# Kernel optimization log

Hardware: AMD Instinct MI355X
Metric: run time of the kernel (lower is better)

Reference implementation:

```python
import jax, jax.numpy as jnp
import numpy as np

DIM = 384
NUM_HEADS = 12
WS = 8            # window_size
SS = 4            # shift_size
HEAD_DIM = DIM // NUM_HEADS
SCALE = HEAD_DIM ** -0.5
N = WS * WS       # tokens per window
EPS = 1e-5
MLP_HIDDEN = 4 * DIM

# relative position index (static, matches torch buffer construction)
_coords = np.stack(np.meshgrid(np.arange(WS), np.arange(WS), indexing='ij')).reshape(2, -1)
_rel = (_coords[:, :, None] - _coords[:, None, :]).transpose(1, 2, 0)  # [N,N,2]
_rel[..., 0] += WS - 1
_rel[..., 1] += WS - 1
_rel[..., 0] *= 2 * WS - 1
RPI = jnp.asarray(_rel.sum(-1))  # [N,N] int


def layer_norm(x, g, b):
    m = x.mean(-1, keepdims=True)
    v = ((x - m) ** 2).mean(-1, keepdims=True)
    return (x - m) / jnp.sqrt(v + EPS) * g + b


def window_partition(x):
    B, Hh, Ww, C = x.shape
    x = x.reshape(B, Hh // WS, WS, Ww // WS, WS, C).transpose(0, 1, 3, 2, 4, 5)
    return x.reshape(-1, WS, WS, C)


def window_reverse(w, Hh, Ww):
    B = w.shape[0] // ((Hh // WS) * (Ww // WS))
    x = w.reshape(B, Hh // WS, Ww // WS, WS, WS, -1).transpose(0, 1, 3, 2, 4, 5)
    return x.reshape(B, Hh, Ww, -1)


def attention_mask(Hp, Wp):
    # region id along each axis: 0 = [0, Hp-WS), 1 = [Hp-WS, Hp-SS), 2 = [Hp-SS, Hp)
    h_id = np.zeros(Hp, np.int32); h_id[Hp - WS:Hp - SS] = 1; h_id[Hp - SS:] = 2
    w_id = np.zeros(Wp, np.int32); w_id[Wp - WS:Wp - SS] = 1; w_id[Wp - SS:] = 2
    cnt = h_id[:, None] * 3 + w_id[None, :]                      # [Hp, Wp]
    img = jnp.asarray(cnt, jnp.float32).reshape(1, Hp, Wp, 1)
    mw = window_partition(img).reshape(-1, N)                    # [nW, N]
    am = mw[:, None, :] - mw[:, :, None]                         # [nW, N, N]
    return jnp.where(am != 0, jnp.float32(-100.0), jnp.float32(0.0))


def setup_inputs() -> dict:
    key = jax.random.key(0)
    ks = jax.random.split(key, 8)
    B, H, W = 32, 64, 64
    std = 0.02
    return {
        'x': jax.random.normal(ks[0], (B, H * W, DIM), jnp.float32),
        'qkv_w': jax.random.normal(ks[1], (DIM, 3 * DIM), jnp.float32) * std,
        'qkv_b': jnp.zeros((3 * DIM,), jnp.float32),
        'proj_w': jax.random.normal(ks[2], (DIM, DIM), jnp.float32) * std,
        'proj_b': jnp.zeros((DIM,), jnp.float32),
        'rpb_table': jax.random.normal(ks[3], ((2 * WS - 1) * (2 * WS - 1), NUM_HEADS), jnp.float32) * std,
        'n1_g': jnp.ones((DIM,), jnp.float32), 'n1_b': jnp.zeros((DIM,), jnp.float32),
        'n2_g': jnp.ones((DIM,), jnp.float32), 'n2_b': jnp.zeros((DIM,), jnp.float32),
        'fc1_w': jax.random.normal(ks[4], (DIM, MLP_HIDDEN), jnp.float32) * std,
        'fc1_b': jnp.zeros((MLP_HIDDEN,), jnp.float32),
        'fc2_w': jax.random.normal(ks[5], (MLP_HIDDEN, DIM), jnp.float32) * std,
        'fc2_b': jnp.zeros((DIM,), jnp.float32),
        'H': 64, 'W': 64,
    }


def reference(x, qkv_w, qkv_b, proj_w, proj_b, rpb_table, n1_g, n1_b, n2_g, n2_b,
              fc1_w, fc1_b, fc2_w, fc2_b, H, W):
    B, L, C = x.shape
    shortcut = x
    h = layer_norm(x, n1_g, n1_b).reshape(B, H, W, C)
    pad_r = (WS - W % WS) % WS
    pad_b = (WS - H % WS) % WS
    if pad_r or pad_b:
        h = jnp.pad(h, ((0, 0), (0, pad_b), (0, pad_r), (0, 0)))
    Hp, Wp = H + pad_b, W + pad_r
    shifted = jnp.roll(h, shift=(-SS, -SS), axis=(1, 2))
    xw = window_partition(shifted).reshape(-1, N, C)             # [B_, N, C]
    B_ = xw.shape[0]

    qkv = (xw @ qkv_w + qkv_b).reshape(B_, N, 3, NUM_HEADS, HEAD_DIM)
    q = qkv[:, :, 0].transpose(0, 2, 1, 3) * SCALE               # [B_, h, N, d]
    k = qkv[:, :, 1].transpose(0, 2, 1, 3)
    v = qkv[:, :, 2].transpose(0, 2, 1, 3)

    attn = jnp.einsum('bhnd,bhmd->bhnm', q, k)                   # [B_, h, N, N]
    bias = rpb_table[RPI].transpose(2, 0, 1)                     # [h, N, N]
    attn = attn + bias[None]

    mask = attention_mask(Hp, Wp)                                # [nW, N, N]
    nW = mask.shape[0]
    attn = attn.reshape(B_ // nW, nW, NUM_HEADS, N, N) + mask[None, :, None]
    attn = jax.nn.softmax(attn.reshape(B_, NUM_HEADS, N, N), axis=-1)

    out = jnp.einsum('bhnm,bhmd->bhnd', attn, v)
    out = out.transpose(0, 2, 1, 3).reshape(B_, N, C)
    out = out @ proj_w + proj_b

    out = window_reverse(out.reshape(-1, WS, WS, C), Hp, Wp)
    out = jnp.roll(out, shift=(SS, SS), axis=(1, 2))
    out = out[:, :H, :W, :].reshape(B, H * W, C)

    x = shortcut + out
    h2 = layer_norm(x, n2_g, n2_b)
    mlp = jax.nn.gelu(h2 @ fc1_w + fc1_b, approximate=False) @ fc2_w + fc2_b
    return x + mlp
```

## Files before the change

kernel.cpp:

```cpp
#include <hip/hip_runtime.h>
#include <math.h>


#define ROWS_TOTAL 131072
#define NWIN_TOTAL 2048

typedef __attribute__((ext_vector_type(8))) __bf16 bf16x8;
typedef __attribute__((ext_vector_type(4))) float f32x4;
typedef __attribute__((ext_vector_type(8))) unsigned short ushort8;

__device__ __forceinline__ unsigned short f2bf(float f) {
  unsigned u = __builtin_bit_cast(unsigned, f);
  u = (u + 0x7fffu + ((u >> 16) & 1u)) >> 16;
  return (unsigned short)u;
}
__device__ __forceinline__ float bf2f(unsigned short u) {
  return __builtin_bit_cast(float, (unsigned)u << 16);
}

__device__ __forceinline__ void gload16(const void* g, void* l) {
  __builtin_amdgcn_global_load_lds(
      (const __attribute__((address_space(1))) unsigned int*)g,
      (__attribute__((address_space(3))) unsigned int*)l, 16, 0, 0);
}

__device__ __forceinline__ int gather_row(int win, int t) {
  int b = win >> 6, wi = (win >> 3) & 7, wj = win & 7;
  int gi = (wi * 8 + (t >> 3) + 4) & 63;
  int gj = (wj * 8 + (t & 7) + 4) & 63;
  return (b << 12) + (gi << 6) + gj;
}

#define LGK0() asm volatile("s_waitcnt lgkmcnt(0)" ::: "memory")
#define VM6() asm volatile("s_waitcnt vmcnt(6)" ::: "memory")
#define VM0() asm volatile("s_waitcnt vmcnt(0)" ::: "memory")
#define SCB() __builtin_amdgcn_sched_barrier(0)
#define BARR() __builtin_amdgcn_s_barrier()
#define PRIO1() __builtin_amdgcn_s_setprio(1)
#define PRIO0() __builtin_amdgcn_s_setprio(0)


#define STGA(b_, c_, kt_)                                                   \
  gload16(aSrcC[c_] + (size_t)(kt_) * 64,                                   \
          (char*)&As[0][0] + (b_) * 32768 + (c_) * 8192 + w * 1024)
#define STGB(b_, c_, kt_)                                                   \
  gload16(bSrcC[c_] + (size_t)(kt_) * 64,                                   \
          (char*)&Bs[0][0] + (b_) * 16384 + (c_) * 8192 + w * 1024)

#define LDA(mi_)                                                            \
  { a[mi_][0] = *(const bf16x8*)(AsB + aOff[mi_][0]);                       \
    a[mi_][1] = *(const bf16x8*)(AsB + aOff[mi_][1]); }
#define LDB(nj_)                                                            \
  { b[nj_][0] = *(const bf16x8*)(BsB + bOff[nj_][0]);                       \
    b[nj_][1] = *(const bf16x8*)(BsB + bOff[nj_][1]); }
#define MM(mi_, nj_)                                                        \
  { acc[mi_][nj_] = __builtin_amdgcn_mfma_f32_16x16x32_bf16(                \
        a[mi_][0], b[nj_][0], acc[mi_][nj_], 0, 0, 0);                      \
    acc[mi_][nj_] = __builtin_amdgcn_mfma_f32_16x16x32_bf16(                \
        a[mi_][1], b[nj_][1], acc[mi_][nj_], 0, 0, 0); }

#define GEMM_DECLS()                                                        \
  f32x4 acc[4][4];                                                          \
  bf16x8 a[4][2], b[4][2];                                                  \
  int aOff[4][2], bOff[4][2];                                               \
  _Pragma("unroll") for (int i_ = 0; i_ < 4; ++i_)                          \
  _Pragma("unroll") for (int j_ = 0; j_ < 4; ++j_)                          \
      acc[i_][j_] = (f32x4)(0.f);                                           \
  _Pragma("unroll") for (int mi_ = 0; mi_ < 4; ++mi_)                       \
  _Pragma("unroll") for (int ks_ = 0; ks_ < 2; ++ks_) {                     \
    int sl_ = ((ks_ * 4 + hi) ^ (lr & 7)) * 8;                              \
    aOff[mi_][ks_] = (wr * 64 + mi_ * 16 + lr) * 64 + sl_;                  \
    bOff[mi_][ks_] = (wc * 64 + mi_ * 16 + lr) * 64 + sl_;                  \
  }

#define GEMM_CORE(NT)                                                       \
  {                                                                         \
    STGA(0, 0, 0); STGA(0, 1, 0); STGA(0, 2, 0); STGA(0, 3, 0);             \
    STGB(0, 0, 0); STGB(0, 1, 0);                                           \
    STGA(1, 0, 1); STGA(1, 1, 1); STGA(1, 2, 1); STGA(1, 3, 1);             \
    STGB(1, 0, 1); STGB(1, 1, 1);                                           \
    VM6(); SCB(); BARR(); SCB();                                            \
    for (int t = 0; t < (NT); ++t) {                                        \
      const int cur = t % 3, nxt = (t + 2) % 3;                             \
      const bool st = (t + 2) < (NT);                                       \
      const int kt = t + 2;                                                 \
      const ushort* AsB = &As[0][0] + cur * 16384;                          \
      const ushort* BsB = &Bs[0][0] + cur * 8192;                           \
                                                                    \
      LDA(0); LDA(1); LDB(0); LDB(1);                                       \
      if (st) { STGA(nxt, 0, kt); STGA(nxt, 1, kt); }                       \
      SCB(); BARR(); LGK0(); SCB();                                         \
      PRIO1(); MM(0, 0); MM(0, 1); MM(1, 0); MM(1, 1); PRIO0();             \
      SCB(); BARR(); SCB();                                                 \
                                                                    \
      LDB(2); LDB(3);                                                       \
      if (st) { STGA(nxt, 2, kt); STGA(nxt, 3, kt); }                       \
      SCB(); BARR(); LGK0(); SCB();                                         \
      PRIO1(); MM(0, 2); MM(0, 3); MM(1, 2); MM(1, 3); PRIO0();             \
      SCB(); BARR(); SCB();                                                 \
                                                                    \
      LDA(2); LDA(3);                                                       \
      if (st) { STGB(nxt, 0, kt); }                                         \
      SCB(); BARR(); LGK0(); SCB();                                         \
      PRIO1(); MM(2, 2); MM(2, 3); MM(3, 2); MM(3, 3); PRIO0();             \
      SCB(); BARR(); SCB();                                                 \
                                                                    \
      if (st) { STGB(nxt, 1, kt); }                                         \
      PRIO1(); MM(2, 0); MM(2, 1); MM(3, 0); MM(3, 1); PRIO0();             \
      if (st) { VM6(); } else { VM0(); }                                    \
      SCB(); BARR(); SCB();                                                 \
    }                                                                       \
  }

__global__ __launch_bounds__(256) void wprep_k(
    const float* __restrict__ qkvw, const float* __restrict__ projw,
    const float* __restrict__ fc1w, const float* __restrict__ fc2w,
    ushort* __restrict__ wq, ushort* __restrict__ wp,
    ushort* __restrict__ w1, ushort* __restrict__ w2) {
  int gid = blockIdx.x * 256 + threadIdx.x;
  const int S1 = 1152 * 384;
  const int S2 = S1 + 384 * 384;
  const int S3 = S2 + 1536 * 384;
  const int S4 = S3 + 384 * 1536;
  if (gid < S1) {
    int n = gid / 384, k = gid - n * 384;
    wq[gid] = f2bf(qkvw[(size_t)k * 1152 + n]);
  } else if (gid < S2) {
    int i = gid - S1, n = i / 384, k = i - n * 384;
    wp[i] = f2bf(projw[(size_t)k * 384 + n]);
  } else if (gid < S3) {
    int i = gid - S2, n = i / 384, k = i - n * 384;
    w1[i] = f2bf(fc1w[(size_t)k * 1536 + n]);
  } else if (gid < S4) {
    int i = gid - S3, n = i / 1536, k = i - n * 1536;
    w2[i] = f2bf(fc2w[(size_t)k * 384 + n]);
  }
}

__global__ __launch_bounds__(256) void ln_fused_k(
    const float* __restrict__ x, const float* __restrict__ g,
    const float* __restrict__ b, ushort* __restrict__ o) {
  int wid = threadIdx.x >> 6, lane = threadIdx.x & 63;
  int row = (blockIdx.x << 2) + wid;
  const float* p = x + (size_t)row * 384;
  float2 v[3];
  float s = 0.f, ss = 0.f;
#pragma unroll
  for (int c = 0; c < 3; ++c) {
    v[c] = *(const float2*)(p + lane * 2 + c * 128);
    s += v[c].x + v[c].y;
    ss += v[c].x * v[c].x + v[c].y * v[c].y;
  }
#pragma unroll
  for (int off = 1; off < 64; off <<= 1) {
    s += __shfl_xor(s, off);
    ss += __shfl_xor(ss, off);
  }
  float m = s * (1.f / 384.f);
  float r = rsqrtf(ss * (1.f / 384.f) - m * m + 1e-5f);
  ushort* op = o + (size_t)row * 384;
#pragma unroll
  for (int c = 0; c < 3; ++c) {
    float2 gg = *(const float2*)(g + lane * 2 + c * 128);
    float2 bb = *(const float2*)(b + lane * 2 + c * 128);
    union { ushort u[2]; unsigned w; } pk;
    pk.u[0] = f2bf((v[c].x - m) * r * gg.x + bb.x);
    pk.u[1] = f2bf((v[c].y - m) * r * gg.y + bb.y);
    *(unsigned*)(op + lane * 2 + c * 128) = pk.w;
  }
}

__global__ __launch_bounds__(512, 2) void qkv_mfma_k(
    const ushort* __restrict__ xln, const ushort* __restrict__ wq,
    const float* __restrict__ qkvb, ushort* __restrict__ qd,
    ushort* __restrict__ kd, ushort* __restrict__ vd, int wc0) {
  __shared__ __align__(16) ushort As[3][16384];
  __shared__ __align__(16) ushort Bs[3][8192];
  __shared__ int rowS[256];
  const int tid = threadIdx.x;
  const int w = tid >> 6, lane = tid & 63;
  const int wr = w >> 1, wc = w & 1;
  int p, bm;
  {
    int lin = blockIdx.y * 9 + blockIdx.x;
    if ((gridDim.y & 7) == 0) {
      int xcd = lin & 7, q = lin >> 3;
      p = q % 9; bm = (q / 9) * 8 + xcd;
    } else { p = blockIdx.x; bm = blockIdx.y; }
  }
  const int n0 = p * 128;
  if (tid < 256) rowS[tid] = gather_row(wc0 + bm * 4 + (tid >> 6), tid & 63);
  __syncthreads();
  const int lr = lane & 15, hi = lane >> 4;
  const int swz = ((tid & 7) ^ ((tid >> 3) & 7)) * 8;
  const ushort* aSrcC[4];
  const ushort* bSrcC[2];
#pragma unroll
  for (int c = 0; c < 4; ++c)
    aSrcC[c] = xln + (size_t)rowS[c * 64 + (tid >> 3)] * 384 + swz;
#pragma unroll
  for (int c = 0; c < 2; ++c)
    bSrcC[c] = wq + (size_t)(n0 + c * 64 + (tid >> 3)) * 384 + swz;
  GEMM_DECLS();
  GEMM_CORE(6);
  const float scale = 0.17677669529663687f;
#pragma unroll
  for (int mi = 0; mi < 4; ++mi) {
#pragma unroll
    for (int r = 0; r < 4; ++r) {
      int rr = wr * 64 + mi * 16 + (hi << 2) + r;
      int w_rel = bm * 4 + (rr >> 6), t = rr & 63;
#pragma unroll
      for (int nj = 0; nj < 4; ++nj) {
        int nc = n0 + wc * 64 + nj * 16 + lr;
        float v = acc[mi][nj][r] + qkvb[nc];
        int qi = nc / 384, rem = nc - qi * 384;
        int hh = rem >> 5, d = rem & 31;
        ushort* base = (qi == 0) ? qd : (qi == 1 ? kd : vd);
        if (qi == 0) v *= scale;
        base[(((size_t)w_rel * 12 + hh) << 11) + (t << 5) + d] = f2bf(v);
      }
    }
  }
}

__global__ __launch_bounds__(128) void attn_k(
    const ushort* __restrict__ q, const ushort* __restrict__ k,
    const ushort* __restrict__ v, const float* __restrict__ rpb,
    ushort* __restrict__ ao, int wc0) {
  __shared__ __align__(16) float kbuf[2][64][32];
  __shared__ __align__(16) float vbuf[2][64][32];
  __shared__ float bias[2][232];
  __shared__ int region[64];
  const int tid = threadIdx.x;
  const int wid = tid >> 6, lane = tid & 63;
  const int w = blockIdx.x, win = wc0 + w;
  const int head = blockIdx.y * 2 + wid;
  if (tid < 64) {
    int wi = (win >> 3) & 7, wj = win & 7;
    int pi = wi * 8 + (tid >> 3), pj = wj * 8 + (tid & 7);
    int ri = pi < 56 ? 0 : (pi < 60 ? 1 : 2);
    int rj = pj < 56 ? 0 : (pj < 60 ? 1 : 2);
    region[tid] = ri * 3 + rj;
  }
  const size_t hb = ((size_t)w * 12 + head) * 2048;
  const ushort* kp = k + hb;
  const ushort* vp = v + hb;
#pragma unroll
  for (int s = 0; s < 4; ++s) {
    int f = s * 64 + lane;
    int r = f >> 2, c = (f & 3) * 8;
    ushort8 ku = *(const ushort8*)(kp + r * 32 + c);
    ushort8 vu = *(const ushort8*)(vp + r * 32 + c);
#pragma unroll
    for (int j = 0; j < 8; ++j) {
      kbuf[wid][r][c + j] = bf2f(ku[j]);
      vbuf[wid][r][c + j] = bf2f(vu[j]);
    }
  }
  for (int s = lane; s < 225; s += 64) bias[wid][s] = rpb[s * 12 + head];
  __syncthreads();
  const int i = lane;
  float qr[32];
  const ushort* qp = q + hb + (i << 5);
#pragma unroll
  for (int c = 0; c < 4; ++c) {
    ushort8 qu = *(const ushort8*)(qp + c * 8);
#pragma unroll
    for (int j = 0; j < 8; ++j) qr[c * 8 + j] = bf2f(qu[j]);
  }
  const int yi = i >> 3, xi = i & 7, regi = region[i];
  float sc[64];
  float mx = -3.0e38f;
#pragma unroll
  for (int j = 0; j < 64; ++j) {
    float a = 0.f;
#pragma unroll
    for (int c = 0; c < 32; c += 4) {
      float4 kv = *(float4*)&kbuf[wid][j][c];
      a = fmaf(qr[c], kv.x, a);
      a = fmaf(qr[c + 1], kv.y, a);
      a = fmaf(qr[c + 2], kv.z, a);
      a = fmaf(qr[c + 3], kv.w, a);
    }
    int dy = yi - (j >> 3) + 7, dx = xi - (j & 7) + 7;
    a += bias[wid][dy * 15 + dx];
    if (region[j] != regi) a -= 100.f;
    sc[j] = a;
    mx = fmaxf(mx, a);
  }
  float sum = 0.f;
#pragma unroll
  for (int j = 0; j < 64; ++j) {
    float e = __expf(sc[j] - mx);
    sc[j] = e;
    sum += e;
  }
  const float inv = 1.f / sum;
  float o[32];
#pragma unroll
  for (int c = 0; c < 32; ++c) o[c] = 0.f;
#pragma unroll
  for (int j = 0; j < 64; ++j) {
    float p = sc[j];
#pragma unroll
    for (int c = 0; c < 32; c += 4) {
      float4 vv = *(float4*)&vbuf[wid][j][c];
      o[c] = fmaf(p, vv.x, o[c]);
      o[c + 1] = fmaf(p, vv.y, o[c + 1]);
      o[c + 2] = fmaf(p, vv.z, o[c + 2]);
      o[c + 3] = fmaf(p, vv.w, o[c + 3]);
    }
  }
  ushort* op = ao + ((size_t)(w * 64 + i)) * 384 + (head << 5);
#pragma unroll
  for (int c = 0; c < 32; c += 8) {
    ushort8 pk;
#pragma unroll
    for (int j2 = 0; j2 < 8; ++j2) pk[j2] = f2bf(o[c + j2] * inv);
    *(ushort8*)(op + c) = pk;
  }
}

__global__ __launch_bounds__(512, 2) void proj_mfma_k(
    const ushort* __restrict__ ao, const ushort* __restrict__ wp,
    const float* __restrict__ pb, const float* __restrict__ x,
    float* __restrict__ x2, int wc0) {
  __shared__ __align__(16) ushort As[3][16384];
  __shared__ __align__(16) ushort Bs[3][8192];
  const int tid = threadIdx.x;
  const int w = tid >> 6, lane = tid & 63;
  const int wr = w >> 1, wc = w & 1;
  int p, bm;
  {
    int lin = blockIdx.y * 3 + blockIdx.x;
    if ((gridDim.y & 7) == 0) {
      int xcd = lin & 7, q = lin >> 3;
      p = q % 3; bm = (q / 3) * 8 + xcd;
    } else { p = blockIdx.x; bm = blockIdx.y; }
  }
  const int n0 = p * 128;
  const int lr = lane & 15, hi = lane >> 4;
  const int swz = ((tid & 7) ^ ((tid >> 3) & 7)) * 8;
  const ushort* aSrcC[4];
  const ushort* bSrcC[2];
#pragma unroll
  for (int c = 0; c < 4; ++c)
    aSrcC[c] = ao + (size_t)(bm * 256 + c * 64 + (tid >> 3)) * 384 + swz;
#pragma unroll
  for (int c = 0; c < 2; ++c)
    bSrcC[c] = wp + (size_t)(n0 + c * 64 + (tid >> 3)) * 384 + swz;
  GEMM_DECLS();
  GEMM_CORE(6);
#pragma unroll
  for (int mi = 0; mi < 4; ++mi) {
#pragma unroll
    for (int r = 0; r < 4; ++r) {
      int rr = wr * 64 + mi * 16 + (hi << 2) + r;
      int gl = bm * 256 + rr;
      int gr = gather_row(wc0 + (gl >> 6), gl & 63);
#pragma unroll
      for (int nj = 0; nj < 4; ++nj) {
        int nc = n0 + wc * 64 + nj * 16 + lr;
        size_t idx = (size_t)gr * 384 + nc;
        x2[idx] = acc[mi][nj][r] + pb[nc] + x[idx];
      }
    }
  }
}

__global__ __launch_bounds__(512, 2) void fc1_mfma_k(
    const ushort* __restrict__ x2ln, const ushort* __restrict__ w1,
    const float* __restrict__ fb, ushort* __restrict__ hm, int row0) {
  __shared__ __align__(16) ushort As[3][16384];
  __shared__ __align__(16) ushort Bs[3][8192];
  const int tid = threadIdx.x;
  const int w = tid >> 6, lane = tid & 63;
  const int wr = w >> 1, wc = w & 1;
  int p, bm;
  {
    int lin = blockIdx.y * 12 + blockIdx.x;
    if ((gridDim.y & 7) == 0) {
      int xcd = lin & 7, q = lin >> 3;
      p = q % 12; bm = (q / 12) * 8 + xcd;
    } else { p = blockIdx.x; bm = blockIdx.y; }
  }
  const int n0 = p * 128;
  const int lr = lane & 15, hi = lane >> 4;
  const int swz = ((tid & 7) ^ ((tid >> 3) & 7)) * 8;
  const ushort* aSrcC[4];
  const ushort* bSrcC[2];
#pragma unroll
  for (int c = 0; c < 4; ++c)
    aSrcC[c] =
        x2ln + (size_t)(row0 + bm * 256 + c * 64 + (tid >> 3)) * 384 + swz;
#pragma unroll
  for (int c = 0; c < 2; ++c)
    bSrcC[c] = w1 + (size_t)(n0 + c * 64 + (tid >> 3)) * 384 + swz;
  GEMM_DECLS();
  GEMM_CORE(6);
#pragma unroll
  for (int mi = 0; mi < 4; ++mi) {
#pragma unroll
    for (int r = 0; r < 4; ++r) {
      int rr = wr * 64 + mi * 16 + (hi << 2) + r;
      size_t lrow = (size_t)(bm * 256 + rr);
#pragma unroll
      for (int nj = 0; nj < 4; ++nj) {
        int nc = n0 + wc * 64 + nj * 16 + lr;
        float v = acc[mi][nj][r] + fb[nc];
        v = 0.5f * v * (1.f + erff(v * 0.70710678118654752f));
        hm[lrow * 1536 + nc] = f2bf(v);
      }
    }
  }
}

__global__ __launch_bounds__(512, 2) void fc2_mfma_k(
    const ushort* __restrict__ hm, const ushort* __restrict__ w2,
    const float* __restrict__ fb, float* __restrict__ out, int row0) {
  __shared__ __align__(16) ushort As[3][16384];
  __shared__ __align__(16) ushort Bs[3][8192];
  const int tid = threadIdx.x;
  const int w = tid >> 6, lane = tid & 63;
  const int wr = w >> 1, wc = w & 1;
  int p, bm;
  {
    int lin = blockIdx.y * 3 + blockIdx.x;
    if ((gridDim.y & 7) == 0) {
      int xcd = lin & 7, q = lin >> 3;
      p = q % 3; bm = (q / 3) * 8 + xcd;
    } else { p = blockIdx.x; bm = blockIdx.y; }
  }
  const int n0 = p * 128;
  const int lr = lane & 15, hi = lane >> 4;
  const int swz = ((tid & 7) ^ ((tid >> 3) & 7)) * 8;
  const ushort* aSrcC[4];
  const ushort* bSrcC[2];
#pragma unroll
  for (int c = 0; c < 4; ++c)
    aSrcC[c] = hm + (size_t)(bm * 256 + c * 64 + (tid >> 3)) * 1536 + swz;
#pragma unroll
  for (int c = 0; c < 2; ++c)
    bSrcC[c] = w2 + (size_t)(n0 + c * 64 + (tid >> 3)) * 1536 + swz;
  GEMM_DECLS();
  GEMM_CORE(24);
#pragma unroll
  for (int mi = 0; mi < 4; ++mi) {
#pragma unroll
    for (int r = 0; r < 4; ++r) {
      int rr = wr * 64 + mi * 16 + (hi << 2) + r;
      size_t grow = (size_t)(row0 + bm * 256 + rr);
#pragma unroll
      for (int nj = 0; nj < 4; ++nj) {
        int nc = n0 + wc * 64 + nj * 16 + lr;
        size_t idx = grow * 384 + nc;
        out[idx] = out[idx] + acc[mi][nj][r] + fb[nc];
      }
    }
  }
}

extern "C" void kernel_launch(void* const* d_in, const int* in_sizes, int n_in,
                              void* d_out, int out_size, void* d_ws, size_t ws_size,
                              hipStream_t stream) {
  const float* x = (const float*)d_in[0];
  const float* qkv_w = (const float*)d_in[1];
  const float* qkv_b = (const float*)d_in[2];
  const float* proj_w = (const float*)d_in[3];
  const float* proj_b = (const float*)d_in[4];
  const float* rpb = (const float*)d_in[5];
  const float* n1g = (const float*)d_in[6];
  const float* n1b = (const float*)d_in[7];
  const float* n2g = (const float*)d_in[8];
  const float* n2b = (const float*)d_in[9];
  const float* fc1w = (const float*)d_in[10];
  const float* fc1b = (const float*)d_in[11];
  const float* fc2w = (const float*)d_in[12];
  const float* fc2b = (const float*)d_in[13];
  float* out = (float*)d_out;
  char* ws = (char*)d_ws;

  ushort* wq = (ushort*)ws;
  ushort* wp = wq + 442368;
  ushort* w1 = wp + 147456;
  ushort* w2 = w1 + 589824;
  ushort* xln = (ushort*)(ws + 3538944);
  char* scratch = ws + 3538944 + 100663296;
  size_t base = 3538944 + 100663296;
  size_t ssz = (ws_size > base) ? ws_size - base : 0;

  wprep_k<<<6912, 256, 0, stream>>>(qkv_w, proj_w, fc1w, fc2w, wq, wp, w1, w2);
  ln_fused_k<<<ROWS_TOTAL / 4, 256, 0, stream>>>(x, n1g, n1b, xln);

  const size_t perwin = 196608;
  int nwc = (int)(ssz / perwin);
  if (nwc > NWIN_TOTAL) nwc = NWIN_TOTAL;
  nwc &= ~3;
  if (nwc < 4) nwc = 4;
  ushort* qd = (ushort*)scratch;
  ushort* kd = qd + (size_t)nwc * 24576;
  ushort* vd = kd + (size_t)nwc * 24576;
  ushort* ao = vd + (size_t)nwc * 24576;
  for (int wc0 = 0; wc0 < NWIN_TOTAL; wc0 += nwc) {
    int nw = (NWIN_TOTAL - wc0 < nwc) ? (NWIN_TOTAL - wc0) : nwc;
    qkv_mfma_k<<<dim3(9, nw / 4), 512, 0, stream>>>(xln, wq, qkv_b, qd, kd, vd, wc0);
    attn_k<<<dim3(nw, 6), 128, 0, stream>>>(qd, kd, vd, rpb, ao, wc0);
    proj_mfma_k<<<dim3(3, nw / 4), 512, 0, stream>>>(ao, wp, proj_b, x, out, wc0);
  }

  ln_fused_k<<<ROWS_TOTAL / 4, 256, 0, stream>>>(out, n2g, n2b, xln);
  const size_t pergrp = 786432;
  int ngc = (int)(ssz / pergrp);
  if (ngc > 512) ngc = 512;
  ngc &= ~7;
  if (ngc < 8) ngc = 8;
  ushort* hm = (ushort*)scratch;
  for (int g0 = 0; g0 < 512; g0 += ngc) {
    int ng = (512 - g0 < ngc) ? (512 - g0) : ngc;
    fc1_mfma_k<<<dim3(12, ng), 512, 0, stream>>>(xln, w1, fc1b, hm, g0 * 256);
    fc2_mfma_k<<<dim3(3, ng), 512, 0, stream>>>(hm, w2, fc2b, out, g0 * 256);
  }
}
```

Baseline: 1.414 ms.

## Retile GEMMs to 256x192 blocks with 2x4 warp grid and double-buffered B

All four MFMA GEMM kernels move from 256x128 output tiles on a 4x2 warp layout to 256x192 tiles on a 2x4 layout. Each warp now holds 128x48 accumulators and reuses B fragments across eight A sub-tiles. B uses a two-stage LDS buffer, A keeps three stages, the pipeline has fewer barriers per k-step, and grid sizes shrink to match. The exact erf in the fc1 GELU is swapped for a polynomial approximation, and the qkv gather-row shared table is replaced by computing the row index directly. The larger accumulator footprint raises register pressure, and the min-blocks hint is dropped, which risks lower occupancy.

```diff
diff --git a/kernel.cpp b/kernel.cpp
--- a/kernel.cpp
+++ b/kernel.cpp
@@ -31,85 +31,134 @@
   return (b << 12) + (gi << 6) + gj;
 }
 
+__device__ __forceinline__ float gelu_f(float v) {
+  float x = v * 0.70710678118654752f;
+  float ax = fabsf(x);
+  float t = 1.f / (1.f + 0.3275911f * ax);
+  float poly =
+      t * (0.254829592f +
+           t * (-0.284496736f +
+                t * (1.421413741f + t * (-1.453152027f + t * 1.061405429f))));
+  float er = 1.f - poly * __expf(-x * x);
+  er = copysignf(er, x);
+  return 0.5f * v * (1.f + er);
+}
+
 #define LGK0() asm volatile("s_waitcnt lgkmcnt(0)" ::: "memory")
-#define VM6() asm volatile("s_waitcnt vmcnt(6)" ::: "memory")
+#define VM4() asm volatile("s_waitcnt vmcnt(4)" ::: "memory")
 #define VM0() asm volatile("s_waitcnt vmcnt(0)" ::: "memory")
 #define SCB() __builtin_amdgcn_sched_barrier(0)
 #define BARR() __builtin_amdgcn_s_barrier()
 #define PRIO1() __builtin_amdgcn_s_setprio(1)
 #define PRIO0() __builtin_amdgcn_s_setprio(0)
 
-
-#define STGA(b_, c_, kt_)                                                   \
-  gload16(aSrcC[c_] + (size_t)(kt_) * 64,                                   \
-          (char*)&As[0][0] + (b_) * 32768 + (c_) * 8192 + w * 1024)
-#define STGB(b_, c_, kt_)                                                   \
-  gload16(bSrcC[c_] + (size_t)(kt_) * 64,                                   \
-          (char*)&Bs[0][0] + (b_) * 16384 + (c_) * 8192 + w * 1024)
-
-#define LDA(mi_)                                                            \
-  { a[mi_][0] = *(const bf16x8*)(AsB + aOff[mi_][0]);                       \
-    a[mi_][1] = *(const bf16x8*)(AsB + aOff[mi_][1]); }
-#define LDB(nj_)                                                            \
-  { b[nj_][0] = *(const bf16x8*)(BsB + bOff[nj_][0]);                       \
-    b[nj_][1] = *(const bf16x8*)(BsB + bOff[nj_][1]); }
-#define MM(mi_, nj_)                                                        \
-  { acc[mi_][nj_] = __builtin_amdgcn_mfma_f32_16x16x32_bf16(                \
-        a[mi_][0], b[nj_][0], acc[mi_][nj_], 0, 0, 0);                      \
-    acc[mi_][nj_] = __builtin_amdgcn_mfma_f32_16x16x32_bf16(                \
-        a[mi_][1], b[nj_][1], acc[mi_][nj_], 0, 0, 0); }
-
-#define GEMM_DECLS()                                                        \
-  f32x4 acc[4][4];                                                          \
-  bf16x8 a[4][2], b[4][2];                                                  \
-  int aOff[4][2], bOff[4][2];                                               \
-  _Pragma("unroll") for (int i_ = 0; i_ < 4; ++i_)                          \
-  _Pragma("unroll") for (int j_ = 0; j_ < 4; ++j_)                          \
-      acc[i_][j_] = (f32x4)(0.f);                                           \
-  _Pragma("unroll") for (int mi_ = 0; mi_ < 4; ++mi_)                       \
-  _Pragma("unroll") for (int ks_ = 0; ks_ < 2; ++ks_) {                     \
-    int sl_ = ((ks_ * 4 + hi) ^ (lr & 7)) * 8;                              \
-    aOff[mi_][ks_] = (wr * 64 + mi_ * 16 + lr) * 64 + sl_;                  \
-    bOff[mi_][ks_] = (wc * 64 + mi_ * 16 + lr) * 64 + sl_;                  \
-  }
-
-#define GEMM_CORE(NT)                                                       \
-  {                                                                         \
-    STGA(0, 0, 0); STGA(0, 1, 0); STGA(0, 2, 0); STGA(0, 3, 0);             \
-    STGB(0, 0, 0); STGB(0, 1, 0);                                           \
-    STGA(1, 0, 1); STGA(1, 1, 1); STGA(1, 2, 1); STGA(1, 3, 1);             \
-    STGB(1, 0, 1); STGB(1, 1, 1);                                           \
-    VM6(); SCB(); BARR(); SCB();                                            \
-    for (int t = 0; t < (NT); ++t) {                                        \
-      const int cur = t % 3, nxt = (t + 2) % 3;                             \
-      const bool st = (t + 2) < (NT);                                       \
-      const int kt = t + 2;                                                 \
-      const ushort* AsB = &As[0][0] + cur * 16384;                          \
-      const ushort* BsB = &Bs[0][0] + cur * 8192;                           \
-                                                                    \
-      LDA(0); LDA(1); LDB(0); LDB(1);                                       \
-      if (st) { STGA(nxt, 0, kt); STGA(nxt, 1, kt); }                       \
-      SCB(); BARR(); LGK0(); SCB();                                         \
-      PRIO1(); MM(0, 0); MM(0, 1); MM(1, 0); MM(1, 1); PRIO0();             \
-      SCB(); BARR(); SCB();                                                 \
-                                                                    \
-      LDB(2); LDB(3);                                                       \
-      if (st) { STGA(nxt, 2, kt); STGA(nxt, 3, kt); }                       \
-      SCB(); BARR(); LGK0(); SCB();                                         \
-      PRIO1(); MM(0, 2); MM(0, 3); MM(1, 2); MM(1, 3); PRIO0();             \
-      SCB(); BARR(); SCB();                                                 \
-                                                                    \
-      LDA(2); LDA(3);                                                       \
-      if (st) { STGB(nxt, 0, kt); }                                         \
-      SCB(); BARR(); LGK0(); SCB();                                         \
-      PRIO1(); MM(2, 2); MM(2, 3); MM(3, 2); MM(3, 3); PRIO0();             \
-      SCB(); BARR(); SCB();                                                 \
-                                                                    \
-      if (st) { STGB(nxt, 1, kt); }                                         \
-      PRIO1(); MM(2, 0); MM(2, 1); MM(3, 0); MM(3, 1); PRIO0();             \
-      if (st) { VM6(); } else { VM0(); }                                    \
-      SCB(); BARR(); SCB();                                                 \
-    }                                                                       \
+#define STGA_(buf_, kt_, c_)                                          \
+  gload16(aSrcC[c_] + (size_t)(kt_) * 64,                             \
+          (char*)As + (buf_) * 32768 + (c_) * 8192 + w * 1024)
+#define STGB_(buf_, kt_, c_)                                          \
+  gload16(bSrcC[c_] + (size_t)(kt_) * 64,                             \
+          (char*)Bs + (buf_) * 24576 + (c_) * 8192 + w * 1024)
+
+#define MM3(mi_, a_, bs_)                                             \
+  { acc[mi_][0] = __builtin_amdgcn_mfma_f32_16x16x32_bf16(            \
+        a_, bs_[0], acc[mi_][0], 0, 0, 0);                            \
+    acc[mi_][1] = __builtin_amdgcn_mfma_f32_16x16x32_bf16(            \
+        a_, bs_[1], acc[mi_][1], 0, 0, 0);                            \
+    acc[mi_][2] = __builtin_amdgcn_mfma_f32_16x16x32_bf16(            \
+        a_, bs_[2], acc[mi_][2], 0, 0, 0); }
+
+#define GEMM_DECLS()                                                  \
+  f32x4 acc[8][3];                                                    \
+  _Pragma("unroll") for (int i_ = 0; i_ < 8; ++i_)                    \
+  _Pragma("unroll") for (int j_ = 0; j_ < 3; ++j_)                    \
+      acc[i_][j_] = (f32x4)(0.f);                                     \
+  const int sl0 = ((hi) ^ (lr & 7)) * 8;                              \
+  const int sl1 = ((4 + hi) ^ (lr & 7)) * 8;                          \
+  const int aB0 = (wr * 128 + lr) * 64 + sl0;                         \
+  const int aB1 = (wr * 128 + lr) * 64 + sl1;                         \
+  const int bB0 = (wc * 48 + lr) * 64 + sl0;                          \
+  const int bB1 = (wc * 48 + lr) * 64 + sl1;
+
+#define GEMM_CORE(NT_)                                                \
+  {                                                                   \
+    STGA_(0, 0, 0); STGA_(0, 0, 1); STGA_(0, 0, 2); STGA_(0, 0, 3);   \
+    STGB_(0, 0, 0); STGB_(0, 0, 1); STGB_(0, 0, 2);                   \
+    STGA_(1, 1, 0); STGA_(1, 1, 1); STGA_(1, 1, 2); STGA_(1, 1, 3);   \
+    VM4(); SCB(); BARR(); SCB();                                      \
+    int curA = 0;                                                     \
+    for (int t = 0; t < (NT_); ++t) {                                 \
+      const int curB = t & 1;                                         \
+      const ushort* AsC = (const ushort*)As + curA * 16384;           \
+      const ushort* BsC = (const ushort*)Bs + curB * 12288;           \
+      if (t + 1 < (NT_)) {                                            \
+        STGB_(curB ^ 1, t + 1, 0);                                    \
+        STGB_(curB ^ 1, t + 1, 1);                                    \
+        STGB_(curB ^ 1, t + 1, 2);                                    \
+      }                                                               \
+      SCB();                                                          \
+      bf16x8 av0, av1, av2, av3, bv0[3], bv1[3];                      \
+      bv0[0] = *(const bf16x8*)(BsC + bB0);                           \
+      bv0[1] = *(const bf16x8*)(BsC + bB0 + 1024);                    \
+      bv0[2] = *(const bf16x8*)(BsC + bB0 + 2048);                    \
+      bv1[0] = *(const bf16x8*)(BsC + bB1);                           \
+      bv1[1] = *(const bf16x8*)(BsC + bB1 + 1024);                    \
+      bv1[2] = *(const bf16x8*)(BsC + bB1 + 2048);                    \
+      av0 = *(const bf16x8*)(AsC + aB0);                              \
+      av1 = *(const bf16x8*)(AsC + aB0 + 1024);                       \
+      av2 = *(const bf16x8*)(AsC + aB0 + 2048);                       \
+      av3 = *(const bf16x8*)(AsC + aB0 + 3072);                       \
+      LGK0(); SCB();                                                  \
+      PRIO1();                                                        \
+      MM3(0, av0, bv0); MM3(1, av1, bv0);                             \
+      MM3(2, av2, bv0); MM3(3, av3, bv0);                             \
+      PRIO0(); SCB();                                                 \
+      av0 = *(const bf16x8*)(AsC + aB1);                              \
+      av1 = *(const bf16x8*)(AsC + aB1 + 1024);                       \
+      av2 = *(const bf16x8*)(AsC + aB1 + 2048);                       \
+      av3 = *(const bf16x8*)(AsC + aB1 + 3072);                       \
+      LGK0(); SCB();                                                  \
+      PRIO1();                                                        \
+      MM3(0, av0, bv1); MM3(1, av1, bv1);                             \
+      MM3(2, av2, bv1); MM3(3, av3, bv1);                             \
+      PRIO0(); SCB();                                                 \
+      if (t + 2 < (NT_)) {                                            \
+        int nbA = curA + 2; if (nbA >= 3) nbA -= 3;                   \
+        STGA_(nbA, t + 2, 0); STGA_(nbA, t + 2, 1);                   \
+        STGA_(nbA, t + 2, 2); STGA_(nbA, t + 2, 3);                   \
+      }                                                               \
+      SCB();                                                          \
+      av0 = *(const bf16x8*)(AsC + aB0 + 4096);                       \
+      av1 = *(const bf16x8*)(AsC + aB0 + 5120);                       \
+      av2 = *(const bf16x8*)(AsC + aB0 + 6144);                       \
+      av3 = *(const bf16x8*)(AsC + aB0 + 7168);                       \
+      LGK0(); SCB();                                                  \
+      PRIO1();                                                        \
+      MM3(4, av0, bv0); MM3(5, av1, bv0);                             \
+      MM3(6, av2, bv0); MM3(7, av3, bv0);                             \
+      PRIO0(); SCB();                                                 \
+      av0 = *(const bf16x8*)(AsC + aB1 + 4096);                       \
+      av1 = *(const bf16x8*)(AsC + aB1 + 5120);                       \
+      av2 = *(const bf16x8*)(AsC + aB1 + 6144);                       \
+      av3 = *(const bf16x8*)(AsC + aB1 + 7168);                       \
+      LGK0(); SCB();                                                  \
+      PRIO1();                                                        \
+      MM3(4, av0, bv1); MM3(5, av1, bv1);                             \
+      MM3(6, av2, bv1); MM3(7, av3, bv1);                             \
+      PRIO0();                                                        \
+      if (t + 2 < (NT_)) { VM4(); SCB(); BARR(); SCB(); }             \
+      else if (t + 1 < (NT_)) { VM0(); SCB(); BARR(); SCB(); }        \
+      ++curA; if (curA == 3) curA = 0;                                \
+    }                                                                 \
+  }
+
+#define GRID_SWZ(NP_)                                                 \
+  int p, bm;                                                          \
+  {                                                                   \
+    int lin = blockIdx.y * (NP_) + blockIdx.x;                        \
+    if ((gridDim.y & 7) == 0) {                                       \
+      int xcd = lin & 7, q = lin >> 3;                                \
+      p = q % (NP_); bm = (q / (NP_)) * 8 + xcd;                      \
+    } else { p = blockIdx.x; bm = blockIdx.y; }                       \
   }
 
 __global__ __launch_bounds__(256) void wprep_k(
@@ -170,49 +219,40 @@
   }
 }
 
-__global__ __launch_bounds__(512, 2) void qkv_mfma_k(
+__global__ __launch_bounds__(512) void qkv_mfma_k(
     const ushort* __restrict__ xln, const ushort* __restrict__ wq,
     const float* __restrict__ qkvb, ushort* __restrict__ qd,
     ushort* __restrict__ kd, ushort* __restrict__ vd, int wc0) {
   __shared__ __align__(16) ushort As[3][16384];
-  __shared__ __align__(16) ushort Bs[3][8192];
-  __shared__ int rowS[256];
+  __shared__ __align__(16) ushort Bs[2][12288];
   const int tid = threadIdx.x;
   const int w = tid >> 6, lane = tid & 63;
-  const int wr = w >> 1, wc = w & 1;
-  int p, bm;
-  {
-    int lin = blockIdx.y * 9 + blockIdx.x;
-    if ((gridDim.y & 7) == 0) {
-      int xcd = lin & 7, q = lin >> 3;
-      p = q % 9; bm = (q / 9) * 8 + xcd;
-    } else { p = blockIdx.x; bm = blockIdx.y; }
-  }
-  const int n0 = p * 128;
-  if (tid < 256) rowS[tid] = gather_row(wc0 + bm * 4 + (tid >> 6), tid & 63);
-  __syncthreads();
+  const int wr = w >> 2, wc = w & 3;
   const int lr = lane & 15, hi = lane >> 4;
-  const int swz = ((tid & 7) ^ ((tid >> 3) & 7)) * 8;
+  GRID_SWZ(6);
+  const int n0 = p * 192;
+  const int sg = ((tid & 7) ^ ((tid >> 3) & 7)) * 8;
   const ushort* aSrcC[4];
-  const ushort* bSrcC[2];
+  const ushort* bSrcC[3];
 #pragma unroll
   for (int c = 0; c < 4; ++c)
-    aSrcC[c] = xln + (size_t)rowS[c * 64 + (tid >> 3)] * 384 + swz;
-#pragma unroll
-  for (int c = 0; c < 2; ++c)
-    bSrcC[c] = wq + (size_t)(n0 + c * 64 + (tid >> 3)) * 384 + swz;
+    aSrcC[c] =
+        xln + (size_t)gather_row(wc0 + bm * 4 + c, tid >> 3) * 384 + sg;
+#pragma unroll
+  for (int c = 0; c < 3; ++c)
+    bSrcC[c] = wq + (size_t)(n0 + c * 64 + (tid >> 3)) * 384 + sg;
   GEMM_DECLS();
   GEMM_CORE(6);
   const float scale = 0.17677669529663687f;
 #pragma unroll
-  for (int mi = 0; mi < 4; ++mi) {
+  for (int mi = 0; mi < 8; ++mi) {
 #pragma unroll
     for (int r = 0; r < 4; ++r) {
-      int rr = wr * 64 + mi * 16 + (hi << 2) + r;
+      int rr = wr * 128 + mi * 16 + (hi << 2) + r;
       int w_rel = bm * 4 + (rr >> 6), t = rr & 63;
 #pragma unroll
-      for (int nj = 0; nj < 4; ++nj) {
-        int nc = n0 + wc * 64 + nj * 16 + lr;
+      for (int nj = 0; nj < 3; ++nj) {
+        int nc = n0 + wc * 48 + nj * 16 + lr;
         float v = acc[mi][nj][r] + qkvb[nc];
         int qi = nc / 384, rem = nc - qi * 384;
         int hh = rem >> 5, d = rem & 31;
@@ -322,46 +362,39 @@
   }
 }
 
-__global__ __launch_bounds__(512, 2) void proj_mfma_k(
+__global__ __launch_bounds__(512) void proj_mfma_k(
     const ushort* __restrict__ ao, const ushort* __restrict__ wp,
     const float* __restrict__ pb, const float* __restrict__ x,
     float* __restrict__ x2, int wc0) {
   __shared__ __align__(16) ushort As[3][16384];
-  __shared__ __align__(16) ushort Bs[3][8192];
+  __shared__ __align__(16) ushort Bs[2][12288];
   const int tid = threadIdx.x;
   const int w = tid >> 6, lane = tid & 63;
-  const int wr = w >> 1, wc = w & 1;
-  int p, bm;
-  {
-    int lin = blockIdx.y * 3 + blockIdx.x;
-    if ((gridDim.y & 7) == 0) {
-      int xcd = lin & 7, q = lin >> 3;
-      p = q % 3; bm = (q / 3) * 8 + xcd;
-    } else { p = blockIdx.x; bm = blockIdx.y; }
-  }
-  const int n0 = p * 128;
+  const int wr = w >> 2, wc = w & 3;
   const int lr = lane & 15, hi = lane >> 4;
-  const int swz = ((tid & 7) ^ ((tid >> 3) & 7)) * 8;
+  GRID_SWZ(2);
+  const int n0 = p * 192;
+  const int sg = ((tid & 7) ^ ((tid >> 3) & 7)) * 8;
   const ushort* aSrcC[4];
-  const ushort* bSrcC[2];
+  const ushort* bSrcC[3];
 #pragma unroll
   for (int c = 0; c < 4; ++c)
-    aSrcC[c] = ao + (size_t)(bm * 256 + c * 64 + (tid >> 3)) * 384 + swz;
-#pragma unroll
-  for (int c = 0; c < 2; ++c)
-    bSrcC[c] = wp + (size_t)(n0 + c * 64 + (tid >> 3)) * 384 + swz;
+    aSrcC[c] = ao + (size_t)(bm * 256 + c * 64 + (tid >> 3)) * 384 + sg;
+#pragma unroll
+  for (int c = 0; c < 3; ++c)
+    bSrcC[c] = wp + (size_t)(n0 + c * 64 + (tid >> 3)) * 384 + sg;
   GEMM_DECLS();
   GEMM_CORE(6);
 #pragma unroll
-  for (int mi = 0; mi < 4; ++mi) {
+  for (int mi = 0; mi < 8; ++mi) {
 #pragma unroll
     for (int r = 0; r < 4; ++r) {
-      int rr = wr * 64 + mi * 16 + (hi << 2) + r;
+      int rr = wr * 128 + mi * 16 + (hi << 2) + r;
       int gl = bm * 256 + rr;
       int gr = gather_row(wc0 + (gl >> 6), gl & 63);
 #pragma unroll
-      for (int nj = 0; nj < 4; ++nj) {
-        int nc = n0 + wc * 64 + nj * 16 + lr;
+      for (int nj = 0; nj < 3; ++nj) {
+        int nc = n0 + wc * 48 + nj * 16 + lr;
         size_t idx = (size_t)gr * 384 + nc;
         x2[idx] = acc[mi][nj][r] + pb[nc] + x[idx];
       }
@@ -369,91 +402,76 @@
   }
 }
 
-__global__ __launch_bounds__(512, 2) void fc1_mfma_k(
+__global__ __launch_bounds__(512) void fc1_mfma_k(
     const ushort* __restrict__ x2ln, const ushort* __restrict__ w1,
     const float* __restrict__ fb, ushort* __restrict__ hm, int row0) {
   __shared__ __align__(16) ushort As[3][16384];
-  __shared__ __align__(16) ushort Bs[3][8192];
+  __shared__ __align__(16) ushort Bs[2][12288];
   const int tid = threadIdx.x;
   const int w = tid >> 6, lane = tid & 63;
-  const int wr = w >> 1, wc = w & 1;
-  int p, bm;
-  {
-    int lin = blockIdx.y * 12 + blockIdx.x;
-    if ((gridDim.y & 7) == 0) {
-      int xcd = lin & 7, q = lin >> 3;
-      p = q % 12; bm = (q / 12) * 8 + xcd;
-    } else { p = blockIdx.x; bm = blockIdx.y; }
-  }
-  const int n0 = p * 128;
+  const int wr = w >> 2, wc = w & 3;
   const int lr = lane & 15, hi = lane >> 4;
-  const int swz = ((tid & 7) ^ ((tid >> 3) & 7)) * 8;
+  GRID_SWZ(8);
+  const int n0 = p * 192;
+  const int sg = ((tid & 7) ^ ((tid >> 3) & 7)) * 8;
   const ushort* aSrcC[4];
-  const ushort* bSrcC[2];
+  const ushort* bSrcC[3];
 #pragma unroll
   for (int c = 0; c < 4; ++c)
     aSrcC[c] =
-        x2ln + (size_t)(row0 + bm * 256 + c * 64 + (tid >> 3)) * 384 + swz;
-#pragma unroll
-  for (int c = 0; c < 2; ++c)
-    bSrcC[c] = w1 + (size_t)(n0 + c * 64 + (tid >> 3)) * 384 + swz;
+        x2ln + (size_t)(row0 + bm * 256 + c * 64 + (tid >> 3)) * 384 + sg;
+#pragma unroll
+  for (int c = 0; c < 3; ++c)
+    bSrcC[c] = w1 + (size_t)(n0 + c * 64 + (tid >> 3)) * 384 + sg;
   GEMM_DECLS();
   GEMM_CORE(6);
 #pragma unroll
-  for (int mi = 0; mi < 4; ++mi) {
+  for (int mi = 0; mi < 8; ++mi) {
 #pragma unroll
     for (int r = 0; r < 4; ++r) {
-      int rr = wr * 64 + mi * 16 + (hi << 2) + r;
+      int rr = wr * 128 + mi * 16 + (hi << 2) + r;
       size_t lrow = (size_t)(bm * 256 + rr);
 #pragma unroll
-      for (int nj = 0; nj < 4; ++nj) {
-        int nc = n0 + wc * 64 + nj * 16 + lr;
-        float v = acc[mi][nj][r] + fb[nc];
-        v = 0.5f * v * (1.f + erff(v * 0.70710678118654752f));
+      for (int nj = 0; nj < 3; ++nj) {
+        int nc = n0 + wc * 48 + nj * 16 + lr;
+        float v = gelu_f(acc[mi][nj][r] + fb[nc]);
         hm[lrow * 1536 + nc] = f2bf(v);
       }
     }
   }
 }
 
-__global__ __launch_bounds__(512, 2) void fc2_mfma_k(
+__global__ __launch_bounds__(512) void fc2_mfma_k(
     const ushort* __restrict__ hm, const ushort* __restrict__ w2,
     const float* __restrict__ fb, float* __restrict__ out, int row0) {
   __shared__ __align__(16) ushort As[3][16384];
-  __shared__ __align__(16) ushort Bs[3][8192];
+  __shared__ __align__(16) ushort Bs[2][12288];
   const int tid = threadIdx.x;
   const int w = tid >> 6, lane = tid & 63;
-  const int wr = w >> 1, wc = w & 1;
-  int p, bm;
-  {
-    int lin = blockIdx.y * 3 + blockIdx.x;
-    if ((gridDim.y & 7) == 0) {
-      int xcd = lin & 7, q = lin >> 3;
-      p = q % 3; bm = (q / 3) * 8 + xcd;
-    } else { p = blockIdx.x; bm = blockIdx.y; }
-  }
-  const int n0 = p * 128;
+  const int wr = w >> 2, wc = w & 3;
   const int lr = lane & 15, hi = lane >> 4;
-  const int swz = ((tid & 7) ^ ((tid >> 3) & 7)) * 8;
+  GRID_SWZ(2);
+  const int n0 = p * 192;
+  const int sg = ((tid & 7) ^ ((tid >> 3) & 7)) * 8;
   const ushort* aSrcC[4];
-  const ushort* bSrcC[2];
+  const ushort* bSrcC[3];
 #pragma unroll
   for (int c = 0; c < 4; ++c)
-    aSrcC[c] = hm + (size_t)(bm * 256 + c * 64 + (tid >> 3)) * 1536 + swz;
-#pragma unroll
-  for (int c = 0; c < 2; ++c)
-    bSrcC[c] = w2 + (size_t)(n0 + c * 64 + (tid >> 3)) * 1536 + swz;
+    aSrcC[c] = hm + (size_t)(bm * 256 + c * 64 + (tid >> 3)) * 1536 + sg;
+#pragma unroll
+  for (int c = 0; c < 3; ++c)
+    bSrcC[c] = w2 + (size_t)(n0 + c * 64 + (tid >> 3)) * 1536 + sg;
   GEMM_DECLS();
   GEMM_CORE(24);
 #pragma unroll
-  for (int mi = 0; mi < 4; ++mi) {
+  for (int mi = 0; mi < 8; ++mi) {
 #pragma unroll
     for (int r = 0; r < 4; ++r) {
-      int rr = wr * 64 + mi * 16 + (hi << 2) + r;
+      int rr = wr * 128 + mi * 16 + (hi << 2) + r;
       size_t grow = (size_t)(row0 + bm * 256 + rr);
 #pragma unroll
-      for (int nj = 0; nj < 4; ++nj) {
-        int nc = n0 + wc * 64 + nj * 16 + lr;
+      for (int nj = 0; nj < 3; ++nj) {
+        int nc = n0 + wc * 48 + nj * 16 + lr;
         size_t idx = grow * 384 + nc;
         out[idx] = out[idx] + acc[mi][nj][r] + fb[nc];
       }
@@ -496,17 +514,19 @@
   const size_t perwin = 196608;
   int nwc = (int)(ssz / perwin);
   if (nwc > NWIN_TOTAL) nwc = NWIN_TOTAL;
-  nwc &= ~3;
-  if (nwc < 4) nwc = 4;
+  nwc &= ~31;
+  if (nwc < 32) nwc = 32;
   ushort* qd = (ushort*)scratch;
   ushort* kd = qd + (size_t)nwc * 24576;
   ushort* vd = kd + (size_t)nwc * 24576;
   ushort* ao = vd + (size_t)nwc * 24576;
   for (int wc0 = 0; wc0 < NWIN_TOTAL; wc0 += nwc) {
     int nw = (NWIN_TOTAL - wc0 < nwc) ? (NWIN_TOTAL - wc0) : nwc;
-    qkv_mfma_k<<<dim3(9, nw / 4), 512, 0, stream>>>(xln, wq, qkv_b, qd, kd, vd, wc0);
+    qkv_mfma_k<<<dim3(6, nw / 4), 512, 0, stream>>>(xln, wq, qkv_b, qd, kd,
+                                                    vd, wc0);
     attn_k<<<dim3(nw, 6), 128, 0, stream>>>(qd, kd, vd, rpb, ao, wc0);
-    proj_mfma_k<<<dim3(3, nw / 4), 512, 0, stream>>>(ao, wp, proj_b, x, out, wc0);
+    proj_mfma_k<<<dim3(2, nw / 4), 512, 0, stream>>>(ao, wp, proj_b, x, out,
+                                                     wc0);
   }
 
   ln_fused_k<<<ROWS_TOTAL / 4, 256, 0, stream>>>(out, n2g, n2b, xln);
@@ -518,7 +538,7 @@
   ushort* hm = (ushort*)scratch;
   for (int g0 = 0; g0 < 512; g0 += ngc) {
     int ng = (512 - g0 < ngc) ? (512 - g0) : ngc;
-    fc1_mfma_k<<<dim3(12, ng), 512, 0, stream>>>(xln, w1, fc1b, hm, g0 * 256);
-    fc2_mfma_k<<<dim3(3, ng), 512, 0, stream>>>(hm, w2, fc2b, out, g0 * 256);
-  }
-}
+    fc1_mfma_k<<<dim3(8, ng), 512, 0, stream>>>(xln, w1, fc1b, hm, g0 * 256);
+    fc2_mfma_k<<<dim3(2, ng), 512, 0, stream>>>(hm, w2, fc2b, out, g0 * 256);
+  }
+}
```

New measurement: 1.373 ms. -2.9%, faster.
